# Kernel optimization log

Measured on AMD Instinct MI355X. Metric: run time of the kernel, lower is better.

## Reference

```python
import jax, jax.numpy as jnp
import numpy as np

SEQ_LEN = 4096
D_MODEL = 1024
NUM_POLES = 64


def setup_inputs() -> dict:
    key = jax.random.key(0)
    k1, k2, k3 = jax.random.split(key, 3)
    z = jax.random.normal(k1, (SEQ_LEN,), dtype=jnp.float32)
    poles = jax.random.normal(k2, (D_MODEL, NUM_POLES), dtype=jnp.float32) * 0.1
    residues = jax.random.normal(k3, (D_MODEL, NUM_POLES), dtype=jnp.float32) * 0.01
    return {"z": z, "poles": poles, "residues": residues}


def reference(z, poles, residues):
    # z: (S,), poles/residues: (D, P) -> out: (S, D)
    # Cauchy sum: out[s, d] = sum_p residues[d, p] / (z[s] - poles[d, p])
    denom = z[:, None, None] - poles[None, :, :]          # (S, D, P)
    result = jnp.sum(residues[None, :, :] / denom, axis=-1)  # (S, D)
    return result
```

## Files before the change

### kernel.cpp

```cpp
#include <hip/hip_runtime.h>
#include <hip/hip_bf16.h>

#define S_TOTAL 4096
#define D_TOTAL 1024
#define NPOLES  64
#define D_PER_BLOCK 64
#define S_PER_BLOCK 32
#define BLOCK 256
#define ZG 8

typedef float f32x2 __attribute__((ext_vector_type(2)));

__device__ __forceinline__ f32x2 splat2(float s) { f32x2 v; v.x = s; v.y = s; return v; }

__device__ __forceinline__ float sanitize_finite(float x) {
    const float lim = 1.0e38f;
    const unsigned u = __float_as_uint(x);
    if ((u & 0x7f800000u) == 0x7f800000u)
        return (u & 0x80000000u) ? -lim : lim;
    return fminf(fmaxf(x, -lim), lim);
}

template <int N>
__device__ __forceinline__ void mergeN(const float* nA, const float* dA,
                                       const float* nB, const float* dB,
                                       float* nO, float* dO) {
#pragma unroll
    for (int k = 0; k < 2 * N; ++k) { dO[k] = 0.f; nO[k] = 0.f; }
#pragma unroll
    for (int i = 0; i < N; ++i)
#pragma unroll
        for (int j = 0; j < N; ++j) {
            dO[i + j] = fmaf(dA[i], dB[j], dO[i + j]);
            nO[i + j] = fmaf(nA[i], dB[j], nO[i + j]);
            nO[i + j] = fmaf(nB[i], dA[j], nO[i + j]);
        }
#pragma unroll
    for (int k = 0; k < N; ++k) {
        dO[N + k] += dA[k] + dB[k];
        nO[N + k] += nA[k] + nB[k];
    }
}

__global__ __launch_bounds__(BLOCK, 4) void cauchy_deg16_kernel(
    const float* __restrict__ z,
    const float* __restrict__ poles,
    const float* __restrict__ residues,
    float* __restrict__ out)
{
    const int tid  = threadIdx.x;
    const int lane = tid & 63;
    const int w    = tid >> 6;
    const int dl   = lane & 15;
    const int q    = lane >> 4;
    const int d0   = blockIdx.y * D_PER_BLOCK;
    const int s0   = blockIdx.x * S_PER_BLOCK;
    const int widx = w * 16 + dl;
    const int myd  = d0 + widx;

    float p[16], r[16];
    {
        const float* pp = poles    + (size_t)myd * NPOLES + q * 16;
        const float* rr = residues + (size_t)myd * NPOLES + q * 16;
#pragma unroll
        for (int k = 0; k < 4; ++k) {
            const float4 p4 = *reinterpret_cast<const float4*>(pp + 4 * k);
            const float4 r4 = *reinterpret_cast<const float4*>(rr + 4 * k);
            p[4 * k + 0] = p4.x; p[4 * k + 1] = p4.y;
            p[4 * k + 2] = p4.z; p[4 * k + 3] = p4.w;
            r[4 * k + 0] = r4.x; r[4 * k + 1] = r4.y;
            r[4 * k + 2] = r4.z; r[4 * k + 3] = r4.w;
        }
    }
    float n1[8][2], d1[8][2];
#pragma unroll
    for (int j = 0; j < 8; ++j) {
        const float pa = p[2 * j], pb = p[2 * j + 1];
        const float ra = r[2 * j], rb = r[2 * j + 1];
        n1[j][1] = ra + rb;
        n1[j][0] = -fmaf(ra, pb, rb * pa);
        d1[j][1] = -(pa + pb);
        d1[j][0] = pa * pb;
    }
    float n2[4][4], d2[4][4];
#pragma unroll
    for (int j = 0; j < 4; ++j)
        mergeN<2>(n1[2 * j], d1[2 * j], n1[2 * j + 1], d1[2 * j + 1], n2[j], d2[j]);
    float n3[2][8], d3[2][8];
#pragma unroll
    for (int j = 0; j < 2; ++j)
        mergeN<4>(n2[2 * j], d2[2 * j], n2[2 * j + 1], d2[2 * j + 1], n3[j], d3[j]);
    float n4[16], d4[16];
    mergeN<8>(n3[0], d3[0], n3[1], d3[1], n4, d4);

    for (int g = 0; g < S_PER_BLOCK / ZG; ++g) {
        const int sb = s0 + g * ZG;
        f32x2 zz[4], acc[4];
#pragma unroll
        for (int t = 0; t < 4; ++t) {
            zz[t].x = z[sb + 2 * t];
            zz[t].y = z[sb + 2 * t + 1];
            acc[t] = splat2(0.f);
        }
#pragma unroll
        for (int t = 0; t < 4; ++t) {
            f32x2 h = zz[t] + splat2(d4[15]);
#pragma unroll
            for (int i = 14; i >= 0; --i)
                h = __builtin_elementwise_fma(h, zz[t], splat2(d4[i]));
            f32x2 n = __builtin_elementwise_fma(splat2(n4[15]), zz[t], splat2(n4[14]));
#pragma unroll
            for (int i = 13; i >= 0; --i)
                n = __builtin_elementwise_fma(n, zz[t], splat2(n4[i]));
            f32x2 rc;
            rc.x = __builtin_amdgcn_rcpf(h.x);
            rc.y = __builtin_amdgcn_rcpf(h.y);
            acc[t] = __builtin_elementwise_fma(n, rc, acc[t]);
        }
#pragma unroll
        for (int t = 0; t < 4; ++t) {
            acc[t].x += __shfl_xor(acc[t].x, 16, 64);
            acc[t].y += __shfl_xor(acc[t].y, 16, 64);
            acc[t].x += __shfl_xor(acc[t].x, 32, 64);
            acc[t].y += __shfl_xor(acc[t].y, 32, 64);
        }
        const float v0 = (q == 0) ? acc[0].x : (q == 1) ? acc[0].y
                       : (q == 2) ? acc[1].x : acc[1].y;
        const float v1 = (q == 0) ? acc[2].x : (q == 1) ? acc[2].y
                       : (q == 2) ? acc[3].x : acc[3].y;
        out[(size_t)(sb + q) * D_TOTAL + myd]     = sanitize_finite(v0);
        out[(size_t)(sb + 4 + q) * D_TOTAL + myd] = sanitize_finite(v1);
    }
}

extern "C" void kernel_launch(void* const* d_in, const int* in_sizes, int n_in,
                              void* d_out, int out_size, void* d_ws, size_t ws_size,
                              hipStream_t stream) {
    const float* z        = (const float*)d_in[0];
    const float* poles    = (const float*)d_in[1];
    const float* residues = (const float*)d_in[2];
    float* out            = (float*)d_out;

    dim3 grid(S_TOTAL / S_PER_BLOCK, D_TOTAL / D_PER_BLOCK);
    dim3 block(BLOCK);
    cauchy_deg16_kernel<<<grid, block, 0, stream>>>(z, poles, residues, out);
}
```

Before: 80.15 us.

## Precompute folded rational coefficients once in a separate kernel, evaluate from workspace

Splits the kernel in two. A small fold kernel builds the degree-16 numerator and denominator polynomial coefficients once per (d, quarter) and writes them to the workspace. The eval kernel stages those coefficients into LDS and runs only the Horner evaluation. This removes the redundant per-block polynomial merging, which was repeated for every s-block, and S_PER_BLOCK is doubled to amortise the coefficient load. The cost is an extra launch and a global round trip for the coefficients.

```diff
diff --git a/kernel.cpp b/kernel.cpp
--- a/kernel.cpp
+++ b/kernel.cpp
@@ -5,7 +5,7 @@
 #define D_TOTAL 1024
 #define NPOLES  64
 #define D_PER_BLOCK 64
-#define S_PER_BLOCK 32
+#define S_PER_BLOCK 64
 #define BLOCK 256
 #define ZG 8
 
@@ -42,35 +42,24 @@
     }
 }
 
-__global__ __launch_bounds__(BLOCK, 4) void cauchy_deg16_kernel(
-    const float* __restrict__ z,
-    const float* __restrict__ poles,
-    const float* __restrict__ residues,
-    float* __restrict__ out)
+__global__ __launch_bounds__(BLOCK) void cauchy_fold_kernel(
+    const float* __restrict__ poles, const float* __restrict__ residues,
+    float4* __restrict__ ws4)
 {
-    const int tid  = threadIdx.x;
-    const int lane = tid & 63;
-    const int w    = tid >> 6;
-    const int dl   = lane & 15;
-    const int q    = lane >> 4;
-    const int d0   = blockIdx.y * D_PER_BLOCK;
-    const int s0   = blockIdx.x * S_PER_BLOCK;
-    const int widx = w * 16 + dl;
-    const int myd  = d0 + widx;
+    const int gid = blockIdx.x * BLOCK + threadIdx.x;
+    const int d = gid >> 2, q = gid & 3;
 
     float p[16], r[16];
-    {
-        const float* pp = poles    + (size_t)myd * NPOLES + q * 16;
-        const float* rr = residues + (size_t)myd * NPOLES + q * 16;
+    const float* pp = poles    + (size_t)d * NPOLES + q * 16;
+    const float* rr = residues + (size_t)d * NPOLES + q * 16;
 #pragma unroll
-        for (int k = 0; k < 4; ++k) {
-            const float4 p4 = *reinterpret_cast<const float4*>(pp + 4 * k);
-            const float4 r4 = *reinterpret_cast<const float4*>(rr + 4 * k);
-            p[4 * k + 0] = p4.x; p[4 * k + 1] = p4.y;
-            p[4 * k + 2] = p4.z; p[4 * k + 3] = p4.w;
-            r[4 * k + 0] = r4.x; r[4 * k + 1] = r4.y;
-            r[4 * k + 2] = r4.z; r[4 * k + 3] = r4.w;
-        }
+    for (int k = 0; k < 4; ++k) {
+        const float4 p4 = *reinterpret_cast<const float4*>(pp + 4 * k);
+        const float4 r4 = *reinterpret_cast<const float4*>(rr + 4 * k);
+        p[4 * k + 0] = p4.x; p[4 * k + 1] = p4.y;
+        p[4 * k + 2] = p4.z; p[4 * k + 3] = p4.w;
+        r[4 * k + 0] = r4.x; r[4 * k + 1] = r4.y;
+        r[4 * k + 2] = r4.z; r[4 * k + 3] = r4.w;
     }
     float n1[8][2], d1[8][2];
 #pragma unroll
@@ -93,6 +82,51 @@
     float n4[16], d4[16];
     mergeN<8>(n3[0], d3[0], n3[1], d3[1], n4, d4);
 
+#pragma unroll
+    for (int j = 0; j < 4; ++j)
+        ws4[(size_t)(j * D_TOTAL + d) * 4 + q] =
+            make_float4(n4[4 * j], n4[4 * j + 1], n4[4 * j + 2], n4[4 * j + 3]);
+#pragma unroll
+    for (int j = 0; j < 4; ++j)
+        ws4[(size_t)((j + 4) * D_TOTAL + d) * 4 + q] =
+            make_float4(d4[4 * j], d4[4 * j + 1], d4[4 * j + 2], d4[4 * j + 3]);
+}
+
+__global__ __launch_bounds__(BLOCK, 4) void cauchy_eval_kernel(
+    const float* __restrict__ z, const float4* __restrict__ ws4,
+    float* __restrict__ out)
+{
+    const int tid  = threadIdx.x;
+    const int lane = tid & 63;
+    const int w    = tid >> 6;
+    const int dl   = lane & 15;
+    const int q    = lane >> 4;
+    const int d0   = blockIdx.y * D_PER_BLOCK;
+    const int s0   = blockIdx.x * S_PER_BLOCK;
+    const int widx = w * 16 + dl;
+    const int myd  = d0 + widx;
+
+    __shared__ float4 cf[8][D_PER_BLOCK][4];
+#pragma unroll
+    for (int j = 0; j < 8; ++j)
+        cf[j][tid >> 2][tid & 3] =
+            ws4[(size_t)(j * D_TOTAL + d0 + (tid >> 2)) * 4 + (tid & 3)];
+    __syncthreads();
+
+    float nr[16], dr[16];
+#pragma unroll
+    for (int j = 0; j < 4; ++j) {
+        const float4 c = cf[j][widx][q];
+        nr[4 * j + 0] = c.x; nr[4 * j + 1] = c.y;
+        nr[4 * j + 2] = c.z; nr[4 * j + 3] = c.w;
+    }
+#pragma unroll
+    for (int j = 0; j < 4; ++j) {
+        const float4 c = cf[j + 4][widx][q];
+        dr[4 * j + 0] = c.x; dr[4 * j + 1] = c.y;
+        dr[4 * j + 2] = c.z; dr[4 * j + 3] = c.w;
+    }
+
     for (int g = 0; g < S_PER_BLOCK / ZG; ++g) {
         const int sb = s0 + g * ZG;
         f32x2 zz[4], acc[4];
@@ -100,22 +134,21 @@
         for (int t = 0; t < 4; ++t) {
             zz[t].x = z[sb + 2 * t];
             zz[t].y = z[sb + 2 * t + 1];
-            acc[t] = splat2(0.f);
         }
 #pragma unroll
         for (int t = 0; t < 4; ++t) {
-            f32x2 h = zz[t] + splat2(d4[15]);
+            f32x2 h = zz[t] + splat2(dr[15]);
 #pragma unroll
             for (int i = 14; i >= 0; --i)
-                h = __builtin_elementwise_fma(h, zz[t], splat2(d4[i]));
-            f32x2 n = __builtin_elementwise_fma(splat2(n4[15]), zz[t], splat2(n4[14]));
+                h = __builtin_elementwise_fma(h, zz[t], splat2(dr[i]));
+            f32x2 n = __builtin_elementwise_fma(splat2(nr[15]), zz[t], splat2(nr[14]));
 #pragma unroll
             for (int i = 13; i >= 0; --i)
-                n = __builtin_elementwise_fma(n, zz[t], splat2(n4[i]));
+                n = __builtin_elementwise_fma(n, zz[t], splat2(nr[i]));
             f32x2 rc;
             rc.x = __builtin_amdgcn_rcpf(h.x);
             rc.y = __builtin_amdgcn_rcpf(h.y);
-            acc[t] = __builtin_elementwise_fma(n, rc, acc[t]);
+            acc[t] = n * rc;
         }
 #pragma unroll
         for (int t = 0; t < 4; ++t) {
@@ -140,8 +173,10 @@
     const float* poles    = (const float*)d_in[1];
     const float* residues = (const float*)d_in[2];
     float* out            = (float*)d_out;
+    float4* ws4           = (float4*)d_ws;
 
+    cauchy_fold_kernel<<<dim3(D_TOTAL * 4 / BLOCK), dim3(BLOCK), 0, stream>>>(
+        poles, residues, ws4);
     dim3 grid(S_TOTAL / S_PER_BLOCK, D_TOTAL / D_PER_BLOCK);
-    dim3 block(BLOCK);
-    cauchy_deg16_kernel<<<grid, block, 0, stream>>>(z, poles, residues, out);
+    cauchy_eval_kernel<<<grid, dim3(BLOCK), 0, stream>>>(z, ws4, out);
 }
```

After: 78.85 us. Within noise of the previous version (-1.6%).
